# Performance work log

Measured on AMD Instinct MI355X. Metric: run time of the kernel, lower is better.

The kernel has to match this reference:

```python
import jax, jax.numpy as jnp
import numpy as np

B, L, H, P, A, T = 64, 256, 1024, 64, 512, 8


def setup_inputs() -> dict:
    key = jax.random.key(0)
    ks = jax.random.split(key, 9)
    return {
        "word_hiddens": jax.random.normal(ks[0], (B, L, H), dtype=jnp.float32),
        "pos_e1_embeddings": jax.random.normal(ks[1], (B, L, P), dtype=jnp.float32),
        "pos_e2_embeddings": jax.random.normal(ks[2], (B, L, P), dtype=jnp.float32),
        "e1_end": jax.random.randint(ks[3], (B,), 0, L, dtype=jnp.int32),
        "e2_end": jax.random.randint(ks[4], (B,), 0, L, dtype=jnp.int32),
        "type_embeddings": jax.random.normal(ks[5], (T, H), dtype=jnp.float32) * 0.03,
        "W_pos": jax.random.normal(ks[6], (H + 2 * P, A), dtype=jnp.float32) * 0.03,
        "W_ent": jax.random.normal(ks[7], (4 * H, A), dtype=jnp.float32) * 0.02,
        "v": jax.random.normal(ks[8], (A,), dtype=jnp.float32) * 0.05,
    }


def _latent_type(e_h, type_emb):
    # alpha = softmax(e_h @ C^T); latent type = alpha @ C   (C: [T, latent])
    scores = jnp.einsum("bh,th->bt", e_h, type_emb)
    alpha = jax.nn.softmax(scores, axis=-1)
    return jnp.einsum("bt,th->bh", alpha, type_emb)


def reference(word_hiddens, pos_e1_embeddings, pos_e2_embeddings, e1_end, e2_end,
              type_embeddings, W_pos, W_ent, v):
    b, seq_len, h = word_hiddens.shape
    batch_idx = jnp.arange(b)
    e1_h = word_hiddens[batch_idx, e1_end]          # [B, H]
    e2_h = word_hiddens[batch_idx, e2_end]          # [B, H]
    e1_type = _latent_type(e1_h, type_embeddings)   # [B, H]
    e2_type = _latent_type(e2_h, type_embeddings)   # [B, H]

    entity_features = jnp.concatenate([e1_h, e1_type, e2_h, e2_type], axis=-1)  # [B, 4H]
    pos_features = jnp.concatenate([word_hiddens, pos_e1_embeddings, pos_e2_embeddings], axis=-1)  # [B, L, H+2P]

    dense_pos = jnp.einsum("blf,fa->bla", pos_features, W_pos)   # [B, L, A]
    dense_ent = entity_features @ W_ent                          # [B, A]
    # Faithful to original tf.repeat(axis=1)+reshape (element-interleaved, not a broadcast)
    dense_ent_r = jnp.repeat(dense_ent, seq_len, axis=1).reshape(b, seq_len, -1)  # [B, L, A]

    u = jnp.tanh(dense_pos + dense_ent_r)            # [B, L, A]
    vu = jnp.einsum("bla,a->bl", u, v)               # [B, L]
    alpha = jax.nn.softmax(vu, axis=-1)              # [B, L]
    z = jnp.einsum("blh,bl->bh", word_hiddens, alpha)  # [B, H]
    return z
```

## Files before the change

### kernel.cpp

```cpp
#include <hip/hip_runtime.h>
#include <hip/hip_bf16.h>
#include <math.h>

#define B_ 64
#define L_ 256
#define H_ 1024
#define P_ 64
#define A_ 512
#define T_ 8
#define NSTEP 36

typedef __attribute__((ext_vector_type(8))) __bf16 bf16x8;
typedef __attribute__((ext_vector_type(4))) float f32x4;

__device__ __forceinline__ float bf2f(ushort u) {
  union { unsigned int i; float f; } v; v.i = ((unsigned int)u) << 16; return v.f;
}
__device__ __forceinline__ ushort f2bf_rne(float f) {
  union { float f; unsigned int i; } v; v.f = f;
  unsigned int r = v.i + 0x7FFFu + ((v.i >> 16) & 1u);
  return (ushort)(r >> 16);
}
__device__ __forceinline__ unsigned int pack2_rne(float a, float b) {
  return (unsigned int)f2bf_rne(a) | ((unsigned int)f2bf_rne(b) << 16);
}

template <bool BF16>
__device__ __forceinline__ float ld1(const void* p, size_t i) {
  if (BF16) return bf2f(((const ushort*)p)[i]);
  return ((const float*)p)[i];
}
template <bool BF16>
__device__ __forceinline__ float4 ld4(const void* p, size_t i) {
  if (BF16) {
    ushort4 u = *(const ushort4*)((const ushort*)p + i);
    return (float4){bf2f(u.x), bf2f(u.y), bf2f(u.z), bf2f(u.w)};
  }
  return *(const float4*)((const float*)p + i);
}

template <bool BF16>
__global__ __launch_bounds__(256) void prep_k(
    const void* __restrict__ wpos, ushort* __restrict__ WTs,
    const void* __restrict__ wh, const int* __restrict__ e1e,
    const int* __restrict__ e2e, const void* __restrict__ temb,
    float* __restrict__ EF) {
  if (blockIdx.x < 576) {
    __shared__ ushort tile[32][33];
    const int s  = blockIdx.x >> 4;
    const int at = blockIdx.x & 15;
    const int tx = threadIdx.x & 31;
    const int ty = threadIdx.x >> 5;
#pragma unroll
    for (int i = 0; i < 4; ++i) {
      size_t idx = (size_t)(s * 32 + ty + i * 8) * A_ + at * 32 + tx;
      ushort u;
      if (BF16) u = ((const ushort*)wpos)[idx];
      else u = f2bf_rne(((const float*)wpos)[idx]);
      tile[ty + i * 8][tx] = u;
    }
    __syncthreads();
#pragma unroll
    for (int i = 0; i < 4; ++i) {
      WTs[(size_t)s * (A_ * 32) + (size_t)(at * 32 + ty + i * 8) * 32 + tx] =
          tile[tx][ty + i * 8];
    }
  } else {
    const int b = blockIdx.x - 576;
    const int tid = threadIdx.x;
    __shared__ float eh1[1024];
    __shared__ float eh2[1024];
    __shared__ float part[256][16];
    __shared__ float scores[16];
    __shared__ float alpha[16];

    const size_t o1 = ((size_t)b * L_ + e1e[b]) * H_;
    const size_t o2 = ((size_t)b * L_ + e2e[b]) * H_;
    for (int h = tid; h < 1024; h += 256) {
      eh1[h] = ld1<BF16>(wh, o1 + h);
      eh2[h] = ld1<BF16>(wh, o2 + h);
    }
    __syncthreads();

    float p[16];
#pragma unroll
    for (int t = 0; t < 16; ++t) p[t] = 0.f;
    for (int h = tid; h < 1024; h += 256) {
      float a1 = eh1[h], a2 = eh2[h];
#pragma unroll
      for (int t = 0; t < 8; ++t) {
        float c = ld1<BF16>(temb, t * 1024 + h);
        p[t] += a1 * c;
        p[8 + t] += a2 * c;
      }
    }
#pragma unroll
    for (int t = 0; t < 16; ++t) part[tid][t] = p[t];
    __syncthreads();
    if (tid < 16) {
      float s = 0.f;
      for (int i = 0; i < 256; ++i) s += part[i][tid];
      scores[tid] = s;
    }
    __syncthreads();
    if (tid < 2) {
      const int base = tid * 8;
      float mx = scores[base];
      for (int t = 1; t < 8; ++t) mx = fmaxf(mx, scores[base + t]);
      float sum = 0.f;
      float e[8];
      for (int t = 0; t < 8; ++t) { e[t] = __expf(scores[base + t] - mx); sum += e[t]; }
      float inv = 1.f / sum;
      for (int t = 0; t < 8; ++t) alpha[base + t] = e[t] * inv;
    }
    __syncthreads();

    float* efb = EF + (size_t)b * 4096;
    for (int h = tid; h < 1024; h += 256) {
      float l1 = 0.f, l2 = 0.f;
#pragma unroll
      for (int t = 0; t < 8; ++t) {
        float c = ld1<BF16>(temb, t * 1024 + h);
        l1 += alpha[t] * c;
        l2 += alpha[8 + t] * c;
      }
      efb[h] = eh1[h];
      efb[1024 + h] = l1;
      efb[2048 + h] = eh2[h];
      efb[3072 + h] = l2;
    }
  }
}

template <bool BF16>
__global__ __launch_bounds__(256) void ent_gemm(const float* __restrict__ EF,
                                                const void* __restrict__ went,
                                                float* __restrict__ part) {
  const int mh = blockIdx.x & 1;
  const int nb = (blockIdx.x >> 1) & 3;
  const int kb = blockIdx.x >> 3;
  const int tid = threadIdx.x;
  __shared__ float efs[32][128];

  const int k0 = kb * 128;
  {
    const int kq = (tid & 31) * 4;
    for (int m = tid >> 5; m < 32; m += 8) {
      *(float4*)&efs[m][kq] = *(const float4*)&EF[(size_t)(mh * 32 + m) * 4096 + k0 + kq];
    }
  }
  __syncthreads();

  const int n0 = nb * 128 + (tid & 31) * 4;
  const int mg = (tid >> 5) * 4;
  float acc[4][4];
#pragma unroll
  for (int i = 0; i < 4; ++i)
#pragma unroll
    for (int j = 0; j < 4; ++j) acc[i][j] = 0.f;

  for (int k = 0; k < 128; ++k) {
    float4 w = ld4<BF16>(went, (size_t)(k0 + k) * A_ + n0);
#pragma unroll
    for (int i = 0; i < 4; ++i) {
      float e = efs[mg + i][k];
      acc[i][0] += e * w.x;
      acc[i][1] += e * w.y;
      acc[i][2] += e * w.z;
      acc[i][3] += e * w.w;
    }
  }
#pragma unroll
  for (int i = 0; i < 4; ++i) {
    *(float4*)&part[((size_t)kb * 64 + mh * 32 + mg + i) * A_ + n0] =
        (float4){acc[i][0], acc[i][1], acc[i][2], acc[i][3]};
  }
}

__global__ __launch_bounds__(256) void ent_reduce(const float* __restrict__ part,
                                                  float* __restrict__ dense_ent) {
  const int idx = blockIdx.x * 256 + threadIdx.x;
  float s = 0.f;
#pragma unroll
  for (int kb = 0; kb < 32; ++kb) s += part[(size_t)kb * 32768 + idx];
  dense_ent[idx] = s;
}

template <bool BF16>
__global__ __launch_bounds__(256, 4) void fused_gemm_vu(
    const void* __restrict__ wh, const void* __restrict__ pe1,
    const void* __restrict__ pe2, const ushort* __restrict__ WTs,
    const float* __restrict__ dense_ent, const void* __restrict__ vvec,
    float* __restrict__ vu_part) {
  __shared__ __align__(16) ushort Abuf[2][64 * 32];
  __shared__ __align__(16) ushort Bbuf[2][128 * 32];
  __shared__ float vu_s[4][64];

  const int tid = threadIdx.x;
  const int pid = blockIdx.x;
  const int wid = (pid & 7) * 128 + (pid >> 3);
  const int nb = wid & 3;
  const int mb = wid >> 2;
  const int rbase = mb * 64;
  const int wave = tid >> 6;
  const int lane = tid & 63;
  const int quad = lane >> 4;
  const int col = lane & 15;
  const int wr = wave >> 1;
  const int wc = wave & 1;

  int aoff[2], boff[4];
#pragma unroll
  for (int mf = 0; mf < 2; ++mf) {
    const int ra = wr * 32 + mf * 16 + col;
    aoff[mf] = ra * 32 + ((quad ^ ((ra >> 1) & 3)) << 3);
  }
#pragma unroll
  for (int nf = 0; nf < 4; ++nf) {
    const int rb = wc * 64 + nf * 16 + col;
    boff[nf] = rb * 32 + ((quad ^ ((rb >> 1) & 3)) << 3);
  }

  const int brow = tid >> 1;
  const int bc0 = (tid & 1) * 2;
  const int sB0 = brow * 32 + ((bc0 ^ ((brow >> 1) & 3)) << 3);
  const size_t bsrc_off = (size_t)(nb * 128 + brow) * 32 + (size_t)(tid & 1) * 16;

  const int ar0 = tid >> 2, aq = tid & 3;
  const int sA0 = ar0 * 32 + ((aq ^ ((ar0 >> 1) & 3)) << 3);

  f32x4 acc[2][4];
#pragma unroll
  for (int i = 0; i < 2; ++i)
#pragma unroll
    for (int j = 0; j < 4; ++j) acc[i][j] = (f32x4){0.f, 0.f, 0.f, 0.f};

  float4 fXa, fXb; uint4 uX; uint4 bX0, bX1;
  float4 fYa, fYb; uint4 uY; uint4 bY0, bY1;

  auto ISSUE_X = [&](int s) {
    const void* src; int ld, k0;
    if (s < 32)      { src = wh;  ld = H_; k0 = s * 32; }
    else if (s < 34) { src = pe1; ld = P_; k0 = (s - 32) * 32; }
    else             { src = pe2; ld = P_; k0 = (s - 34) * 32; }
    if (BF16) {
      uX = *(const uint4*)((const ushort*)src + (size_t)(rbase + ar0) * ld + k0 + aq * 8);
    } else {
      const float* p0 = (const float*)src + (size_t)(rbase + ar0) * ld + k0 + aq * 8;
      fXa = *(const float4*)p0;
      fXb = *(const float4*)(p0 + 4);
    }
    const ushort* bs = WTs + (size_t)s * (A_ * 32) + bsrc_off;
    bX0 = *(const uint4*)bs;
    bX1 = *(const uint4*)(bs + 8);
  };
  auto ISSUE_Y = [&](int s) {
    const void* src; int ld, k0;
    if (s < 32)      { src = wh;  ld = H_; k0 = s * 32; }
    else if (s < 34) { src = pe1; ld = P_; k0 = (s - 32) * 32; }
    else             { src = pe2; ld = P_; k0 = (s - 34) * 32; }
    if (BF16) {
      uY = *(const uint4*)((const ushort*)src + (size_t)(rbase + ar0) * ld + k0 + aq * 8);
    } else {
      const float* p0 = (const float*)src + (size_t)(rbase + ar0) * ld + k0 + aq * 8;
      fYa = *(const float4*)p0;
      fYb = *(const float4*)(p0 + 4);
    }
    const ushort* bs = WTs + (size_t)s * (A_ * 32) + bsrc_off;
    bY0 = *(const uint4*)bs;
    bY1 = *(const uint4*)(bs + 8);
  };
  auto STORE_X = [&](int buf) {
    if (BF16) {
      *(uint4*)&Abuf[buf][sA0] = uX;
    } else {
      uint4 u0 = {pack2_rne(fXa.x, fXa.y), pack2_rne(fXa.z, fXa.w),
                  pack2_rne(fXb.x, fXb.y), pack2_rne(fXb.z, fXb.w)};
      *(uint4*)&Abuf[buf][sA0] = u0;
    }
    *(uint4*)&Bbuf[buf][sB0] = bX0;
    *(uint4*)&Bbuf[buf][sB0 ^ 8] = bX1;
  };
  auto STORE_Y = [&](int buf) {
    if (BF16) {
      *(uint4*)&Abuf[buf][sA0] = uY;
    } else {
      uint4 u0 = {pack2_rne(fYa.x, fYa.y), pack2_rne(fYa.z, fYa.w),
                  pack2_rne(fYb.x, fYb.y), pack2_rne(fYb.z, fYb.w)};
      *(uint4*)&Abuf[buf][sA0] = u0;
    }
    *(uint4*)&Bbuf[buf][sB0] = bY0;
    *(uint4*)&Bbuf[buf][sB0 ^ 8] = bY1;
  };
  auto COMPUTE = [&](int buf) {
    bf16x8 af[2], bfr[4];
#pragma unroll
    for (int mf = 0; mf < 2; ++mf) af[mf] = *(const bf16x8*)&Abuf[buf][aoff[mf]];
#pragma unroll
    for (int nf = 0; nf < 4; ++nf) bfr[nf] = *(const bf16x8*)&Bbuf[buf][boff[nf]];
#pragma unroll
    for (int mf = 0; mf < 2; ++mf)
#pragma unroll
      for (int nf = 0; nf < 4; ++nf)
        acc[mf][nf] =
            __builtin_amdgcn_mfma_f32_16x16x32_bf16(af[mf], bfr[nf], acc[mf][nf], 0, 0, 0);
  };

  ISSUE_X(0);
  ISSUE_Y(1);
  STORE_X(0);
  __syncthreads();

  for (int s = 0; s < NSTEP; s += 2) {
    if (s + 2 < NSTEP) ISSUE_X(s + 2);
    COMPUTE(0);
    STORE_Y(1);
    __syncthreads();
    if (s + 3 < NSTEP) ISSUE_Y(s + 3);
    COMPUTE(1);
    if (s + 2 < NSTEP) {
      STORE_X(0);
      __syncthreads();
    }
  }

  float vv[4];
#pragma unroll
  for (int nf = 0; nf < 4; ++nf)
    vv[nf] = ld1<BF16>(vvec, nb * 128 + wc * 64 + nf * 16 + col);

#pragma unroll
  for (int mf = 0; mf < 2; ++mf) {
    const int row0 = wr * 32 + mf * 16 + quad * 4;
    const int r0 = rbase + row0;
    const int bidx = r0 >> 8;
    const int l0 = r0 & 255;
    const float* ebase = dense_ent + bidx * A_ + 2 * l0 + (nb >> 1);
    float e0 = ebase[0], e1 = ebase[2], e2 = ebase[4], e3 = ebase[6];
    float s0 = 0.f, s1 = 0.f, s2 = 0.f, s3 = 0.f;
#pragma unroll
    for (int nf = 0; nf < 4; ++nf) {
      float vn = vv[nf];
      s0 += tanhf(acc[mf][nf][0] + e0) * vn;
      s1 += tanhf(acc[mf][nf][1] + e1) * vn;
      s2 += tanhf(acc[mf][nf][2] + e2) * vn;
      s3 += tanhf(acc[mf][nf][3] + e3) * vn;
    }
    s0 += __shfl_xor(s0, 1); s0 += __shfl_xor(s0, 2); s0 += __shfl_xor(s0, 4); s0 += __shfl_xor(s0, 8);
    s1 += __shfl_xor(s1, 1); s1 += __shfl_xor(s1, 2); s1 += __shfl_xor(s1, 4); s1 += __shfl_xor(s1, 8);
    s2 += __shfl_xor(s2, 1); s2 += __shfl_xor(s2, 2); s2 += __shfl_xor(s2, 4); s2 += __shfl_xor(s2, 8);
    s3 += __shfl_xor(s3, 1); s3 += __shfl_xor(s3, 2); s3 += __shfl_xor(s3, 4); s3 += __shfl_xor(s3, 8);
    if (col == 0) {
      vu_s[wave][row0 + 0] = s0;
      vu_s[wave][row0 + 1] = s1;
      vu_s[wave][row0 + 2] = s2;
      vu_s[wave][row0 + 3] = s3;
    }
  }
  __syncthreads();
  if (tid < 64) {
    const int wrr = tid >> 5;
    float s = vu_s[wrr * 2][tid] + vu_s[wrr * 2 + 1][tid];
    vu_part[(size_t)nb * (B_ * L_) + rbase + tid] = s;
  }
}

template <bool BF16>
__global__ __launch_bounds__(256) void softmax_z(const void* __restrict__ wh,
                                                 const float* __restrict__ vu_part,
                                                 void* __restrict__ out) {
  const int b = blockIdx.x >> 2;
  const int hq = blockIdx.x & 3;
  const int tid = threadIdx.x;
  __shared__ float alpha[256];
  __shared__ float red[256];

  float x = 0.f;
#pragma unroll
  for (int p = 0; p < 4; ++p) x += vu_part[(size_t)p * (B_ * L_) + b * L_ + tid];
  red[tid] = x;
  __syncthreads();
  for (int s = 128; s > 0; s >>= 1) {
    if (tid < s) red[tid] = fmaxf(red[tid], red[tid + s]);
    __syncthreads();
  }
  float m = red[0];
  __syncthreads();
  float e = __expf(x - m);
  red[tid] = e;
  __syncthreads();
  for (int s = 128; s > 0; s >>= 1) {
    if (tid < s) red[tid] += red[tid + s];
    __syncthreads();
  }
  alpha[tid] = e / red[0];
  __syncthreads();

  const int h = hq * 256 + tid;
  const size_t base = (size_t)b * L_ * H_ + h;
  float a0 = 0.f, a1 = 0.f, a2 = 0.f, a3 = 0.f;
  float a4 = 0.f, a5 = 0.f, a6 = 0.f, a7 = 0.f;
  for (int l = 0; l < 256; l += 8) {
    a0 += alpha[l + 0] * ld1<BF16>(wh, base + (size_t)(l + 0) * H_);
    a1 += alpha[l + 1] * ld1<BF16>(wh, base + (size_t)(l + 1) * H_);
    a2 += alpha[l + 2] * ld1<BF16>(wh, base + (size_t)(l + 2) * H_);
    a3 += alpha[l + 3] * ld1<BF16>(wh, base + (size_t)(l + 3) * H_);
    a4 += alpha[l + 4] * ld1<BF16>(wh, base + (size_t)(l + 4) * H_);
    a5 += alpha[l + 5] * ld1<BF16>(wh, base + (size_t)(l + 5) * H_);
    a6 += alpha[l + 6] * ld1<BF16>(wh, base + (size_t)(l + 6) * H_);
    a7 += alpha[l + 7] * ld1<BF16>(wh, base + (size_t)(l + 7) * H_);
  }
  float z = ((a0 + a1) + (a2 + a3)) + ((a4 + a5) + (a6 + a7));
  if (BF16) ((ushort*)out)[b * H_ + h] = f2bf_rne(z);
  else ((float*)out)[b * H_ + h] = z;
}

extern "C" void kernel_launch(void* const* d_in, const int* in_sizes, int n_in,
                              void* d_out, int out_size, void* d_ws, size_t ws_size,
                              hipStream_t stream) {
  const void* wh   = d_in[0];
  const void* pe1  = d_in[1];
  const void* pe2  = d_in[2];
  const int*  e1e  = (const int*)d_in[3];
  const int*  e2e  = (const int*)d_in[4];
  const void* temb = d_in[5];
  const void* wpos = d_in[6];
  const void* went = d_in[7];
  const void* vvec = d_in[8];

  const bool bf16 = (in_sizes[0] == (int)(B_ * L_ * H_ * 2));

  char* ws = (char*)d_ws;
  ushort* WTs      = (ushort*)ws;
  float* dense_ent = (float*)(ws + 1179648);
  float* vu_part   = (float*)(ws + 1310720);
  float* EF        = (float*)(ws + 1310720);
  float* part      = (float*)(ws + 2359296);

  if (bf16) {
    prep_k<true ><<<dim3(640), dim3(256), 0, stream>>>(wpos, WTs, wh, e1e, e2e, temb, EF);
    ent_gemm<true ><<<dim3(256), dim3(256), 0, stream>>>(EF, went, part);
    ent_reduce<<<dim3(128), dim3(256), 0, stream>>>(part, dense_ent);
    fused_gemm_vu<true ><<<dim3(1024), dim3(256), 0, stream>>>(wh, pe1, pe2, WTs, dense_ent, vvec, vu_part);
    softmax_z<true ><<<dim3(256), dim3(256), 0, stream>>>(wh, vu_part, d_out);
  } else {
    prep_k<false><<<dim3(640), dim3(256), 0, stream>>>(wpos, WTs, wh, e1e, e2e, temb, EF);
    ent_gemm<false><<<dim3(256), dim3(256), 0, stream>>>(EF, went, part);
    ent_reduce<<<dim3(128), dim3(256), 0, stream>>>(part, dense_ent);
    fused_gemm_vu<false><<<dim3(1024), dim3(256), 0, stream>>>(wh, pe1, pe2, WTs, dense_ent, vvec, vu_part);
    softmax_z<false><<<dim3(256), dim3(256), 0, stream>>>(wh, vu_part, d_out);
  }
}
```

Before: 189.4 us.

## Use non-draining barriers in GEMM loop, vectorize softmax_z, tree-reduce type scores

The main GEMM pipeline swaps __syncthreads for a custom barrier that waits only on LDS counters (lgkmcnt). Outstanding global prefetch loads can then stay in flight across the barrier instead of being drained. softmax_z now has each thread handle two adjacent H columns with paired loads, using half as many blocks, which cuts the redundant per-block softmax recomputation. The entity-type score reduction in prep_k becomes a two-level reduction instead of a serial 256-element loop. The custom barrier relies on STORE_X/STORE_Y having consumed their global loads already, and fewer softmax blocks lowers parallelism.

```diff
diff --git a/kernel.cpp b/kernel.cpp
--- a/kernel.cpp
+++ b/kernel.cpp
@@ -31,12 +31,28 @@
   return ((const float*)p)[i];
 }
 template <bool BF16>
+__device__ __forceinline__ float2 ld2(const void* p, size_t i) {
+  if (BF16) {
+    ushort2 u = *(const ushort2*)((const ushort*)p + i);
+    return (float2){bf2f(u.x), bf2f(u.y)};
+  }
+  return *(const float2*)((const float*)p + i);
+}
+template <bool BF16>
 __device__ __forceinline__ float4 ld4(const void* p, size_t i) {
   if (BF16) {
     ushort4 u = *(const ushort4*)((const ushort*)p + i);
     return (float4){bf2f(u.x), bf2f(u.y), bf2f(u.z), bf2f(u.w)};
   }
   return *(const float4*)((const float*)p + i);
+}
+
+__device__ __forceinline__ void barrier_nodrain() {
+  __builtin_amdgcn_sched_barrier(0);
+  asm volatile("s_waitcnt lgkmcnt(0)" ::: "memory");
+  __builtin_amdgcn_sched_barrier(0);
+  __builtin_amdgcn_s_barrier();
+  __builtin_amdgcn_sched_barrier(0);
 }
 
 template <bool BF16>
@@ -71,6 +87,7 @@
     __shared__ float eh1[1024];
     __shared__ float eh2[1024];
     __shared__ float part[256][16];
+    __shared__ float part2[16][17];
     __shared__ float scores[16];
     __shared__ float alpha[16];
 
@@ -97,9 +114,18 @@
 #pragma unroll
     for (int t = 0; t < 16; ++t) part[tid][t] = p[t];
     __syncthreads();
+    {
+      const int t = tid & 15, j = tid >> 4;
+      float s = 0.f;
+#pragma unroll
+      for (int i = 0; i < 16; ++i) s += part[j * 16 + i][t];
+      part2[j][t] = s;
+    }
+    __syncthreads();
     if (tid < 16) {
       float s = 0.f;
-      for (int i = 0; i < 256; ++i) s += part[i][tid];
+#pragma unroll
+      for (int i = 0; i < 16; ++i) s += part2[i][tid];
       scores[tid] = s;
     }
     __syncthreads();
@@ -309,18 +335,18 @@
   ISSUE_X(0);
   ISSUE_Y(1);
   STORE_X(0);
-  __syncthreads();
+  barrier_nodrain();
 
   for (int s = 0; s < NSTEP; s += 2) {
     if (s + 2 < NSTEP) ISSUE_X(s + 2);
     COMPUTE(0);
     STORE_Y(1);
-    __syncthreads();
+    barrier_nodrain();
     if (s + 3 < NSTEP) ISSUE_Y(s + 3);
     COMPUTE(1);
     if (s + 2 < NSTEP) {
       STORE_X(0);
-      __syncthreads();
+      barrier_nodrain();
     }
   }
 
@@ -369,8 +395,8 @@
 __global__ __launch_bounds__(256) void softmax_z(const void* __restrict__ wh,
                                                  const float* __restrict__ vu_part,
                                                  void* __restrict__ out) {
-  const int b = blockIdx.x >> 2;
-  const int hq = blockIdx.x & 3;
+  const int b = blockIdx.x >> 1;
+  const int hh = blockIdx.x & 1;
   const int tid = threadIdx.x;
   __shared__ float alpha[256];
   __shared__ float red[256];
@@ -396,23 +422,30 @@
   alpha[tid] = e / red[0];
   __syncthreads();
 
-  const int h = hq * 256 + tid;
-  const size_t base = (size_t)b * L_ * H_ + h;
-  float a0 = 0.f, a1 = 0.f, a2 = 0.f, a3 = 0.f;
-  float a4 = 0.f, a5 = 0.f, a6 = 0.f, a7 = 0.f;
+  const int h0 = hh * 512 + tid * 2;
+  const size_t base = (size_t)b * L_ * H_ + h0;
+  float z0 = 0.f, z1 = 0.f;
   for (int l = 0; l < 256; l += 8) {
-    a0 += alpha[l + 0] * ld1<BF16>(wh, base + (size_t)(l + 0) * H_);
-    a1 += alpha[l + 1] * ld1<BF16>(wh, base + (size_t)(l + 1) * H_);
-    a2 += alpha[l + 2] * ld1<BF16>(wh, base + (size_t)(l + 2) * H_);
-    a3 += alpha[l + 3] * ld1<BF16>(wh, base + (size_t)(l + 3) * H_);
-    a4 += alpha[l + 4] * ld1<BF16>(wh, base + (size_t)(l + 4) * H_);
-    a5 += alpha[l + 5] * ld1<BF16>(wh, base + (size_t)(l + 5) * H_);
-    a6 += alpha[l + 6] * ld1<BF16>(wh, base + (size_t)(l + 6) * H_);
-    a7 += alpha[l + 7] * ld1<BF16>(wh, base + (size_t)(l + 7) * H_);
-  }
-  float z = ((a0 + a1) + (a2 + a3)) + ((a4 + a5) + (a6 + a7));
-  if (BF16) ((ushort*)out)[b * H_ + h] = f2bf_rne(z);
-  else ((float*)out)[b * H_ + h] = z;
+    float2 u0 = ld2<BF16>(wh, base + (size_t)(l + 0) * H_);
+    float2 u1 = ld2<BF16>(wh, base + (size_t)(l + 1) * H_);
+    float2 u2 = ld2<BF16>(wh, base + (size_t)(l + 2) * H_);
+    float2 u3 = ld2<BF16>(wh, base + (size_t)(l + 3) * H_);
+    float2 u4 = ld2<BF16>(wh, base + (size_t)(l + 4) * H_);
+    float2 u5 = ld2<BF16>(wh, base + (size_t)(l + 5) * H_);
+    float2 u6 = ld2<BF16>(wh, base + (size_t)(l + 6) * H_);
+    float2 u7 = ld2<BF16>(wh, base + (size_t)(l + 7) * H_);
+    float a0 = alpha[l + 0], a1 = alpha[l + 1], a2 = alpha[l + 2], a3 = alpha[l + 3];
+    float a4 = alpha[l + 4], a5 = alpha[l + 5], a6 = alpha[l + 6], a7 = alpha[l + 7];
+    z0 += a0 * u0.x + a1 * u1.x + a2 * u2.x + a3 * u3.x
+        + a4 * u4.x + a5 * u5.x + a6 * u6.x + a7 * u7.x;
+    z1 += a0 * u0.y + a1 * u1.y + a2 * u2.y + a3 * u3.y
+        + a4 * u4.y + a5 * u5.y + a6 * u6.y + a7 * u7.y;
+  }
+  if (BF16) {
+    ((unsigned int*)out)[((size_t)b * H_ + h0) >> 1] = pack2_rne(z0, z1);
+  } else {
+    *(float2*)((float*)out + (size_t)b * H_ + h0) = (float2){z0, z1};
+  }
 }
 
 extern "C" void kernel_launch(void* const* d_in, const int* in_sizes, int n_in,
@@ -442,12 +475,12 @@
     ent_gemm<true ><<<dim3(256), dim3(256), 0, stream>>>(EF, went, part);
     ent_reduce<<<dim3(128), dim3(256), 0, stream>>>(part, dense_ent);
     fused_gemm_vu<true ><<<dim3(1024), dim3(256), 0, stream>>>(wh, pe1, pe2, WTs, dense_ent, vvec, vu_part);
-    softmax_z<true ><<<dim3(256), dim3(256), 0, stream>>>(wh, vu_part, d_out);
+    softmax_z<true ><<<dim3(128), dim3(256), 0, stream>>>(wh, vu_part, d_out);
   } else {
     prep_k<false><<<dim3(640), dim3(256), 0, stream>>>(wpos, WTs, wh, e1e, e2e, temb, EF);
     ent_gemm<false><<<dim3(256), dim3(256), 0, stream>>>(EF, went, part);
     ent_reduce<<<dim3(128), dim3(256), 0, stream>>>(part, dense_ent);
     fused_gemm_vu<false><<<dim3(1024), dim3(256), 0, stream>>>(wh, pe1, pe2, WTs, dense_ent, vvec, vu_part);
-    softmax_z<false><<<dim3(256), dim3(256), 0, stream>>>(wh, vu_part, d_out);
-  }
-}
+    softmax_z<false><<<dim3(128), dim3(256), 0, stream>>>(wh, vu_part, d_out);
+  }
+}
```

Measured after the change: 190.0 us. No clear change (+0.3%).
